# Performance work log

Hardware: AMD Instinct MI355X
Metric: run time of the kernel (lower is better)

## Reference

```python
import jax, jax.numpy as jnp
import numpy as np

B, S, F = 2, 2048, 2048
H, D = 16, 128  # F == H * D


def setup_inputs() -> dict:
    key = jax.random.key(0)
    k1, k2, k3 = jax.random.split(key, 3)
    x = jax.random.normal(k1, (B, S, F), dtype=jnp.float32)
    # causal attention mask, broadcast over batch and heads
    mask = jnp.tril(jnp.ones((S, S), dtype=bool))[None, None, :, :]
    init_std = 0.02
    c_attn_kernel = jax.random.normal(k2, (F, 3 * F), dtype=jnp.float32) * init_std
    c_attn_bias = jnp.zeros((3 * F,), dtype=jnp.float32)
    c_proj_kernel = jax.random.normal(k3, (F, F), dtype=jnp.float32) * init_std
    c_proj_bias = jnp.zeros((F,), dtype=jnp.float32)
    return {
        "x": x,
        "mask": mask,
        "c_attn_kernel": c_attn_kernel,
        "c_attn_bias": c_attn_bias,
        "c_proj_kernel": c_proj_kernel,
        "c_proj_bias": c_proj_bias,
    }


def reference(x, mask, c_attn_kernel, c_attn_bias, c_proj_kernel, c_proj_bias):
    dtype = x.dtype
    # fused QKV projection: [B,S,F] @ [F,3F] -> [B,S,3F]
    hidden = jnp.einsum('bsf,fe->bse', x, c_attn_kernel) + c_attn_bias
    q, k, v = jnp.split(hidden, 3, axis=-1)
    split = lambda t: t.reshape(t.shape[:-1] + (H, D))  # [B,S,H,D]
    q, k, v = split(q), split(k), split(v)
    q = q / jnp.sqrt(jnp.asarray(D, dtype))
    scores = jnp.einsum('bqhd,bkhd->bhqk', q, k)  # [B,H,S,S]
    big_neg = jnp.finfo(dtype).min
    scores = jnp.where(mask[..., :S, :S], scores, big_neg)
    weights = jax.nn.softmax(scores, axis=-1)
    z = jnp.einsum('bhqk,bkhd->bqhd', weights, v)  # [B,S,H,D]
    merged = z.reshape(z.shape[:-2] + (F,))  # [B,S,F]
    out = jnp.einsum('bsf,fe->bse', merged, c_proj_kernel) + c_proj_bias
    return out
```

## Files before the change

### kernel.cpp

```cpp
#include <hip/hip_runtime.h>
#include <hip/hip_bf16.h>
#include <stdint.h>

typedef __attribute__((ext_vector_type(8))) __bf16 bf16x8;
typedef __attribute__((ext_vector_type(4))) __bf16 bf16x4;
typedef __attribute__((ext_vector_type(4))) float f32x4;

#define DEV __device__ __forceinline__

static constexpr int S = 2048, F = 2048, H = 16, D = 128;
static constexpr int KDIM = F;
static constexpr float QSCALE = 0.08838834764831845f;

DEV void gll16(const void* g, void* l) {
  __builtin_amdgcn_global_load_lds(
      (const __attribute__((address_space(1))) void*)g,
      (__attribute__((address_space(3))) void*)l, 16, 0, 0);
}

DEV f32x4 mfma16(bf16x8 a, bf16x8 b, f32x4 c) {
  return __builtin_amdgcn_mfma_f32_16x16x32_bf16(a, b, c, 0, 0, 0);
}

extern __shared__ char smem[];

__global__ void k_cvt(const float* __restrict__ in, __bf16* __restrict__ out) {
  int i = blockIdx.x * 256 + threadIdx.x;
  float4 v = reinterpret_cast<const float4*>(in)[i];
  bf16x4 o = {(__bf16)v.x, (__bf16)v.y, (__bf16)v.z, (__bf16)v.w};
  reinterpret_cast<bf16x4*>(out)[i] = o;
}

__global__ void k_transpose(const float* __restrict__ in, __bf16* __restrict__ out,
                            int rows, int cols) {
  __shared__ float t[64][65];
  const int c0 = blockIdx.x * 64, r0 = blockIdx.y * 64;
  const int tx = threadIdx.x & 63, ty = threadIdx.x >> 6;
#pragma unroll
  for (int i = 0; i < 64; i += 4)
    t[ty + i][tx] = in[(size_t)(r0 + ty + i) * cols + c0 + tx];
  __syncthreads();
#pragma unroll
  for (int i = 0; i < 64; i += 4)
    out[(size_t)(c0 + ty + i) * rows + r0 + tx] = (__bf16)t[tx][ty + i];
}

template <int BM, int BN, int NBXL, int EPI>
__global__ __launch_bounds__(512, 1) void k_gp(
    const __bf16* __restrict__ A, const __bf16* __restrict__ Bt,
    const float* __restrict__ bias,
    __bf16* __restrict__ qo, __bf16* __restrict__ ko, __bf16* __restrict__ vo,
    float* __restrict__ fo) {
  constexpr int MF = BM / 32;
  constexpr int NF = BN / 64;
  constexpr int NH = NF / 2;
  constexpr int NLA = BM / 64;
  constexpr int NLB = BN / 64;
  constexpr int NL = NLA + NLB;
  constexpr int AOFF = BM * 128;
  constexpr int BUFSZ = (BM + BN) * 128;
  constexpr int NT = KDIM / 64;

  const int tid = threadIdx.x;
  const int lane = tid & 63, wid = tid >> 6;
  const int wm = wid >> 2, wn = wid & 3;
  const int ln = lane & 15, lm = lane >> 4;

  const int q8 = gridDim.x >> 3;
  const int lin = (blockIdx.x & 7) * q8 + (blockIdx.x >> 3);
  const int by = lin >> NBXL, bx = lin & ((1 << NBXL) - 1);
  const int mBase = by * BM, nBase = bx * BN;

  const int r0 = tid >> 3, cc = tid & 7;
  const int src0 = r0 * KDIM + ((cc ^ (r0 & 7)) << 3);
  const __bf16* Ab = A + (size_t)mBase * KDIM + src0;
  const __bf16* Bb = Bt + (size_t)nBase * KDIM + src0;
  const int dstBase = wid * 1024;

  auto stage = [&](char* buf, int t) {
    const __bf16* As = Ab + t * 64;
    const __bf16* Bs = Bb + t * 64;
#pragma unroll
    for (int j = 0; j < NLA; ++j)
      gll16(As + (size_t)j * 64 * KDIM, buf + j * 8192 + dstBase);
#pragma unroll
    for (int j = 0; j < NLB; ++j)
      gll16(Bs + (size_t)j * 64 * KDIM, buf + AOFF + j * 8192 + dstBase);
  };
  auto wait_nl = [&]() {
    if constexpr (NL == 4)       asm volatile("s_waitcnt vmcnt(4)" ::: "memory");
    else if constexpr (NL == 6)  asm volatile("s_waitcnt vmcnt(6)" ::: "memory");
    else if constexpr (NL == 8)  asm volatile("s_waitcnt vmcnt(8)" ::: "memory");
    else                         asm volatile("s_waitcnt vmcnt(10)" ::: "memory");
  };

  int rA[2], rB[2];
#pragma unroll
  for (int ks = 0; ks < 2; ++ks) {
    const int slot = (ks * 4 + lm) ^ (ln & 7);
    rA[ks] = (wm * (BM / 2) + ln) * 128 + slot * 16;
    rB[ks] = AOFF + (wn * (BN / 4) + ln) * 128 + slot * 16;
  }

  f32x4 acc[MF][NF] = {};

  stage(smem, 0);
  stage(smem + BUFSZ, 1);
  wait_nl();
  __builtin_amdgcn_s_barrier();
  __builtin_amdgcn_sched_barrier(0);

  for (int t = 0; t < NT; ++t) {
    char* cb = smem + (t & 1) * BUFSZ;
    bf16x8 a0[MF], a1[MF], b0[NF], b1[NF];

#pragma unroll
    for (int mi = 0; mi < MF; ++mi)
      a0[mi] = *reinterpret_cast<const bf16x8*>(cb + rA[0] + mi * 2048);
#pragma unroll
    for (int ni = 0; ni < NH; ++ni)
      b0[ni] = *reinterpret_cast<const bf16x8*>(cb + rB[0] + ni * 2048);
#pragma unroll
    for (int ni = NH; ni < NF; ++ni)
      b0[ni] = *reinterpret_cast<const bf16x8*>(cb + rB[0] + ni * 2048);

    __builtin_amdgcn_s_setprio(1);
#pragma unroll
    for (int ni = 0; ni < NH; ++ni)
#pragma unroll
      for (int mi = 0; mi < MF; ++mi)
        acc[mi][ni] = mfma16(a0[mi], b0[ni], acc[mi][ni]);
    __builtin_amdgcn_s_setprio(0);

#pragma unroll
    for (int mi = 0; mi < MF; ++mi)
      a1[mi] = *reinterpret_cast<const bf16x8*>(cb + rA[1] + mi * 2048);
#pragma unroll
    for (int ni = NH; ni < NF; ++ni)
      b1[ni] = *reinterpret_cast<const bf16x8*>(cb + rB[1] + ni * 2048);

    __builtin_amdgcn_s_setprio(1);
#pragma unroll
    for (int ni = NH; ni < NF; ++ni)
#pragma unroll
      for (int mi = 0; mi < MF; ++mi)
        acc[mi][ni] = mfma16(a0[mi], b0[ni], acc[mi][ni]);
    __builtin_amdgcn_s_setprio(0);

#pragma unroll
    for (int ni = 0; ni < NH; ++ni)
      b1[ni] = *reinterpret_cast<const bf16x8*>(cb + rB[1] + ni * 2048);

    __builtin_amdgcn_s_setprio(1);
#pragma unroll
    for (int ni = NH; ni < NF; ++ni)
#pragma unroll
      for (int mi = 0; mi < MF; ++mi)
        acc[mi][ni] = mfma16(a1[mi], b1[ni], acc[mi][ni]);
    __builtin_amdgcn_s_setprio(0);

    asm volatile("s_waitcnt lgkmcnt(0)" ::: "memory");
    __builtin_amdgcn_s_barrier();
    __builtin_amdgcn_sched_barrier(0);
    if (t + 2 < NT) stage(cb, t + 2);

    __builtin_amdgcn_s_setprio(1);
#pragma unroll
    for (int ni = 0; ni < NH; ++ni)
#pragma unroll
      for (int mi = 0; mi < MF; ++mi)
        acc[mi][ni] = mfma16(a1[mi], b1[ni], acc[mi][ni]);
    __builtin_amdgcn_s_setprio(0);

    if (t + 2 < NT) {
      wait_nl();
    } else if (t + 1 < NT) {
      asm volatile("s_waitcnt vmcnt(0)" ::: "memory");
    }
    if (t + 1 < NT) {
      __builtin_amdgcn_s_barrier();
      __builtin_amdgcn_sched_barrier(0);
    }
  }

  if (EPI == 0) {
#pragma unroll
    for (int mi = 0; mi < MF; ++mi) {
      const int grow = mBase + wm * (BM / 2) + mi * 16 + lm * 4;
      const int b = grow >> 11, s0 = grow & 2047;
#pragma unroll
      for (int ni = 0; ni < NF; ++ni) {
        const int gcol = nBase + wn * (BN / 4) + ni * 16 + ln;
        const float bv = bias[gcol];
        const int sec = gcol >> 11;
        const int h = (gcol >> 7) & 15, d = gcol & 127;
        const int bh = b * H + h;
        if (sec == 0) {
#pragma unroll
          for (int r = 0; r < 4; ++r)
            qo[((size_t)bh * S + s0 + r) * D + d] = (__bf16)((acc[mi][ni][r] + bv) * QSCALE);
        } else if (sec == 1) {
#pragma unroll
          for (int r = 0; r < 4; ++r)
            ko[((size_t)bh * S + s0 + r) * D + d] = (__bf16)(acc[mi][ni][r] + bv);
        } else {
          bf16x4 pv = {(__bf16)(acc[mi][ni][0] + bv), (__bf16)(acc[mi][ni][1] + bv),
                       (__bf16)(acc[mi][ni][2] + bv), (__bf16)(acc[mi][ni][3] + bv)};
          *reinterpret_cast<bf16x4*>(vo + ((size_t)bh * D + d) * S + s0) = pv;
        }
      }
    }
  } else {
#pragma unroll
    for (int mi = 0; mi < MF; ++mi) {
      const int grow = mBase + wm * (BM / 2) + mi * 16 + lm * 4;
#pragma unroll
      for (int ni = 0; ni < NF; ++ni) {
        const int gcol = nBase + wn * (BN / 4) + ni * 16 + ln;
        const float bv = bias[gcol];
#pragma unroll
        for (int r = 0; r < 4; ++r)
          fo[(size_t)(grow + r) * F + gcol] = acc[mi][ni][r] + bv;
      }
    }
  }
}

__global__ __launch_bounds__(256, 2) void k_attn(
    const __bf16* __restrict__ qb, const __bf16* __restrict__ kb,
    const __bf16* __restrict__ vtb, __bf16* __restrict__ zb) {
  const int lane = threadIdx.x & 63, w = threadIdx.x >> 6;
  const int lm = lane >> 4, ln = lane & 15;
  const int blk = blockIdx.x;
  const int u = blk & 255, v = blk >> 8;
  const int qt = v ? (u >> 4) : 15 - (u >> 4);
  const int bh = ((u & 15) << 1) | v;
  const int qw = qt * 128 + w * 32;

  const __bf16* qp = qb + (size_t)bh * S * D;
  const __bf16* kp = kb + (size_t)bh * S * D;
  const __bf16* vp = vtb + (size_t)bh * D * S;
  char* pw = smem + 65536 + w * 4096;

  int ksrc[4], kdst[4], vsrc[4], vdst[4];
#pragma unroll
  for (int j = 0; j < 4; ++j) {
    int c = (w * 4 + j) * 64 + lane;
    int kr = c >> 4, kps = (c & 15) ^ (kr & 7);
    ksrc[j] = kr * D + kps * 8;
    kdst[j] = (w * 4 + j) * 1024;
    int vr = c >> 3, vps = (c & 7) ^ (vr & 7);
    vsrc[j] = vr * S + vps * 8;
    vdst[j] = 16384 + (w * 4 + j) * 1024;
  }

  bf16x8 qf[2][4];
#pragma unroll
  for (int mi = 0; mi < 2; ++mi)
#pragma unroll
    for (int kf = 0; kf < 4; ++kf)
      qf[mi][kf] = *reinterpret_cast<const bf16x8*>(qp + (qw + mi * 16 + ln) * D + kf * 32 + lm * 8);

  f32x4 Oa[2][8] = {};
  float mrow[2][4], lrow[2][4];
#pragma unroll
  for (int mi = 0; mi < 2; ++mi)
#pragma unroll
    for (int r = 0; r < 4; ++r) { mrow[mi][r] = -3.0e38f; lrow[mi][r] = 0.0f; }

  const int ktEnd = 2 * qt + 1;

#pragma unroll
  for (int j = 0; j < 4; ++j) gll16(kp + ksrc[j], smem + kdst[j]);
#pragma unroll
  for (int j = 0; j < 4; ++j) gll16(vp + vsrc[j], smem + vdst[j]);
  asm volatile("s_waitcnt vmcnt(0)" ::: "memory");
  __builtin_amdgcn_s_barrier();
  __builtin_amdgcn_sched_barrier(0);

  for (int kt = 0; kt <= ktEnd; ++kt) {
    const int kv0 = kt * 64;
    const int cur = kt & 1;

    if (kt < ktEnd) {
      const int nk = (kt + 1) * 64;
      char* nbuf = smem + (cur ^ 1) * 32768;
#pragma unroll
      for (int j = 0; j < 4; ++j) gll16(kp + (size_t)nk * D + ksrc[j], nbuf + kdst[j]);
#pragma unroll
      for (int j = 0; j < 4; ++j) gll16(vp + nk + vsrc[j], nbuf + vdst[j]);
    }

    if (kv0 <= qw + 31) {
      const char* Kb = smem + cur * 32768;
      const char* Vb = Kb + 16384;
      const bool diag = (kv0 + 63 > qw);

      f32x4 sacc[2][4] = {};
#pragma unroll
      for (int kf = 0; kf < 4; ++kf) {
        bf16x8 kfr[4];
#pragma unroll
        for (int ni = 0; ni < 4; ++ni) {
          int row = ni * 16 + ln;
          int ch = (kf * 4 + lm) ^ (row & 7);
          kfr[ni] = *reinterpret_cast<const bf16x8*>(Kb + row * 256 + ch * 16);
        }
        __builtin_amdgcn_s_setprio(1);
#pragma unroll
        for (int mi = 0; mi < 2; ++mi)
#pragma unroll
          for (int ni = 0; ni < 4; ++ni)
            sacc[mi][ni] = mfma16(qf[mi][kf], kfr[ni], sacc[mi][ni]);
        __builtin_amdgcn_s_setprio(0);
      }

      if (diag) {
#pragma unroll
        for (int ni = 0; ni < 4; ++ni) {
          int c = kv0 + ni * 16 + ln;
#pragma unroll
          for (int mi = 0; mi < 2; ++mi) {
            int q0r = qw + mi * 16 + lm * 4;
#pragma unroll
            for (int r = 0; r < 4; ++r)
              if (c > q0r + r) sacc[mi][ni][r] = -1e30f;
          }
        }
      }

#pragma unroll
      for (int mi = 0; mi < 2; ++mi)
#pragma unroll
        for (int r = 0; r < 4; ++r) {
          float mx = fmaxf(fmaxf(sacc[mi][0][r], sacc[mi][1][r]),
                           fmaxf(sacc[mi][2][r], sacc[mi][3][r]));
          mx = fmaxf(mx, __shfl_xor(mx, 1, 64));
          mx = fmaxf(mx, __shfl_xor(mx, 2, 64));
          mx = fmaxf(mx, __shfl_xor(mx, 4, 64));
          mx = fmaxf(mx, __shfl_xor(mx, 8, 64));
          float mnew = fmaxf(mrow[mi][r], mx);
          float corr = __expf(mrow[mi][r] - mnew);
          mrow[mi][r] = mnew;
          float rs = 0.0f;
#pragma unroll
          for (int ni = 0; ni < 4; ++ni) {
            float p = __expf(sacc[mi][ni][r] - mnew);
            sacc[mi][ni][r] = p;
            rs += p;
          }
          lrow[mi][r] = lrow[mi][r] * corr + rs;
#pragma unroll
          for (int ni = 0; ni < 8; ++ni) Oa[mi][ni][r] *= corr;
        }

#pragma unroll
      for (int mi = 0; mi < 2; ++mi)
#pragma unroll
        for (int ni = 0; ni < 4; ++ni)
#pragma unroll
          for (int r = 0; r < 4; ++r) {
            int row = mi * 16 + lm * 4 + r;
            int bo = (row * 128 + (ni * 16 + ln) * 2) ^ ((row & 7) << 4);
            *reinterpret_cast<__bf16*>(pw + bo) = (__bf16)sacc[mi][ni][r];
          }

      asm volatile("s_waitcnt lgkmcnt(0)" ::: "memory");
      __builtin_amdgcn_sched_barrier(0);

#pragma unroll
      for (int kf = 0; kf < 2; ++kf) {
        bf16x8 pfr[2], vfr[8];
#pragma unroll
        for (int mi = 0; mi < 2; ++mi) {
          int row = mi * 16 + ln;
          int ch = (kf * 4 + lm) ^ (row & 7);
          pfr[mi] = *reinterpret_cast<const bf16x8*>(pw + row * 128 + ch * 16);
        }
#pragma unroll
        for (int ni = 0; ni < 8; ++ni) {
          int row = ni * 16 + ln;
          int ch = (kf * 4 + lm) ^ (row & 7);
          vfr[ni] = *reinterpret_cast<const bf16x8*>(Vb + row * 128 + ch * 16);
        }
        __builtin_amdgcn_s_setprio(1);
#pragma unroll
        for (int mi = 0; mi < 2; ++mi)
#pragma unroll
          for (int ni = 0; ni < 8; ++ni)
            Oa[mi][ni] = mfma16(pfr[mi], vfr[ni], Oa[mi][ni]);
        __builtin_amdgcn_s_setprio(0);
      }
    }

    asm volatile("s_waitcnt vmcnt(0) lgkmcnt(0)" ::: "memory");
    __builtin_amdgcn_s_barrier();
    __builtin_amdgcn_sched_barrier(0);
  }

#pragma unroll
  for (int mi = 0; mi < 2; ++mi)
#pragma unroll
    for (int r = 0; r < 4; ++r) {
      float ls = lrow[mi][r];
      ls += __shfl_xor(ls, 1, 64);
      ls += __shfl_xor(ls, 2, 64);
      ls += __shfl_xor(ls, 4, 64);
      ls += __shfl_xor(ls, 8, 64);
      lrow[mi][r] = 1.0f / ls;
    }
  const int b = bh >> 4, h = bh & 15;
#pragma unroll
  for (int mi = 0; mi < 2; ++mi)
#pragma unroll
    for (int ni = 0; ni < 8; ++ni) {
      int d = ni * 16 + ln;
#pragma unroll
      for (int r = 0; r < 4; ++r) {
        int qrow = qw + mi * 16 + lm * 4 + r;
        zb[(size_t)(b * S + qrow) * F + h * D + d] = (__bf16)(Oa[mi][ni][r] * lrow[mi][r]);
      }
    }
}

extern "C" void kernel_launch(void* const* d_in, const int* in_sizes, int n_in,
                              void* d_out, int out_size, void* d_ws, size_t ws_size,
                              hipStream_t stream) {
  const float* x = (const float*)d_in[0];
  const float* w_attn = (const float*)d_in[2];
  const float* b_attn = (const float*)d_in[3];
  const float* w_proj = (const float*)d_in[4];
  const float* b_proj = (const float*)d_in[5];
  float* out = (float*)d_out;

  char* ws = (char*)d_ws;
  __bf16* xb    = (__bf16*)(ws + 0);
  __bf16* wqkv  = (__bf16*)(ws + 16777216);
  __bf16* wpro  = (__bf16*)(ws + 41943040);
  __bf16* qb    = (__bf16*)(ws + 50331648);
  __bf16* kb    = (__bf16*)(ws + 67108864);
  __bf16* vtb   = (__bf16*)(ws + 83886080);
  __bf16* zb    = xb;

  (void)hipFuncSetAttribute((const void*)k_gp<128, 384, 4, 0>,
                            hipFuncAttributeMaxDynamicSharedMemorySize, 131072);
  (void)hipFuncSetAttribute((const void*)k_gp<128, 256, 3, 1>,
                            hipFuncAttributeMaxDynamicSharedMemorySize, 98304);
  (void)hipFuncSetAttribute((const void*)k_attn,
                            hipFuncAttributeMaxDynamicSharedMemorySize, 81920);

  k_cvt<<<8192, 256, 0, stream>>>(x, xb);
  k_transpose<<<dim3(96, 32), 256, 0, stream>>>(w_attn, wqkv, 2048, 6144);
  k_transpose<<<dim3(32, 32), 256, 0, stream>>>(w_proj, wpro, 2048, 2048);
  k_gp<128, 384, 4, 0><<<512, 512, 131072, stream>>>(xb, wqkv, b_attn, qb, kb, vtb, nullptr);
  k_attn<<<512, 256, 81920, stream>>>(qb, kb, vtb, zb);
  k_gp<128, 256, 3, 1><<<256, 512, 98304, stream>>>(zb, wpro, b_proj, nullptr, nullptr, nullptr, out);
}
```

Measured before the change: 258.9 us.

## Add 256x256-tile QKV GEMM with 8-phase interleaved load/MFMA schedule

Replaces the QKV projection GEMM (previously 128x384 tiles, 512 blocks) with a dedicated kernel using 256x256 tiles over 384 blocks. Global-to-LDS loads are split into half-tile pieces, and each piece is issued between MFMA phases with fine-grained barriers and vmcnt waits, so loads overlap compute across a double buffer. The larger tile raises operand reuse per LDS read, and 384 blocks avoids a partial second wave. The cost is more barriers per K step and a hand-tuned wait-count schedule that is fragile. The rest of the changes are macro refactors and removal of the now-unused epilogue template parameter.

```diff
diff --git a/kernel.cpp b/kernel.cpp
--- a/kernel.cpp
+++ b/kernel.cpp
@@ -45,12 +45,172 @@
     out[(size_t)(c0 + ty + i) * rows + r0 + tx] = (__bf16)t[tx][ty + i];
 }
 
-template <int BM, int BN, int NBXL, int EPI>
+template <int MH>
+DEV void mmq(f32x4 (&acc)[8][4], const bf16x8 (&a)[4], const bf16x8 (&b)[4]) {
+#pragma unroll
+  for (int ni = 0; ni < 4; ++ni)
+#pragma unroll
+    for (int mi = 0; mi < 4; ++mi)
+      acc[MH * 4 + mi][ni] = mfma16(a[mi], b[ni], acc[MH * 4 + mi][ni]);
+}
+
+#define QBAR()  __builtin_amdgcn_s_barrier()
+#define QLGKM() asm volatile("s_waitcnt lgkmcnt(0)" ::: "memory")
+#define QSCB()  __builtin_amdgcn_sched_barrier(0)
+
+__global__ __launch_bounds__(512, 1) void k_qkv8(
+    const __bf16* __restrict__ A, const __bf16* __restrict__ Bt,
+    const float* __restrict__ bias,
+    __bf16* __restrict__ qo, __bf16* __restrict__ ko, __bf16* __restrict__ vo) {
+  constexpr int NT = 32;
+
+  const int tid = threadIdx.x;
+  const int lane = tid & 63, wid = tid >> 6;
+  const int wm = wid >> 2, wn = wid & 3;
+  const int ln = lane & 15, lm = lane >> 4;
+
+  const int lin = (blockIdx.x & 7) * 48 + (blockIdx.x >> 3);
+  const int by = lin / 24, bx = lin % 24;
+  const int mBase = by * 256, nBase = bx * 256;
+
+  const int r0 = tid >> 3, cc = tid & 7;
+  const int src0 = r0 * KDIM + ((cc ^ (r0 & 7)) << 3);
+  const __bf16* Ab = A + (size_t)mBase * KDIM + src0;
+  const __bf16* Bb = Bt + (size_t)nBase * KDIM + src0;
+  const int sDst = wid * 1024;
+
+  auto stA = [&](int t, int h) {
+    char* d = smem + (t & 1) * 65536 + h * 16384 + sDst;
+    const __bf16* s = Ab + (size_t)(h * 128) * KDIM + t * 64;
+    gll16(s, d);
+    gll16(s + (size_t)64 * KDIM, d + 8192);
+  };
+  auto stB = [&](int t, int h) {
+    char* d = smem + (t & 1) * 65536 + 32768 + h * 16384 + sDst;
+    const __bf16* s = Bb + (size_t)(h * 128) * KDIM + t * 64;
+    gll16(s, d);
+    gll16(s + (size_t)64 * KDIM, d + 8192);
+  };
+
+  int aOff[2], bOff[2];
+#pragma unroll
+  for (int ks = 0; ks < 2; ++ks) {
+    const int slot = (ks * 4 + lm) ^ (ln & 7);
+    aOff[ks] = (wm * 128 + ln) * 128 + slot * 16;
+    bOff[ks] = 32768 + (wn * 64 + ln) * 128 + slot * 16;
+  }
+  auto rdA = [&](bf16x8 (&a)[4], const char* rb, int mh, int ks) {
+#pragma unroll
+    for (int mi = 0; mi < 4; ++mi)
+      a[mi] = *reinterpret_cast<const bf16x8*>(rb + aOff[ks] + (mh * 4 + mi) * 2048);
+  };
+  auto rdB = [&](bf16x8 (&b)[4], const char* rb, int ks) {
+#pragma unroll
+    for (int ni = 0; ni < 4; ++ni)
+      b[ni] = *reinterpret_cast<const bf16x8*>(rb + bOff[ks] + ni * 2048);
+  };
+
+  f32x4 acc[8][4] = {};
+
+  stA(0, 0); stA(0, 1); stB(0, 0); stB(0, 1); stB(1, 0);
+  asm volatile("s_waitcnt vmcnt(2)" ::: "memory");
+  QBAR(); QSCB();
+
+  for (int i = 0; i < 16; ++i) {
+    const char* L = smem;
+    const char* R = smem + 65536;
+    const int t1 = 2 * i + 1, t2 = 2 * i + 2, t3 = 2 * i + 3;
+    const bool last = (i == 15);
+    bf16x8 a[4], b0[4], b1[4];
+
+    rdA(a, L, 0, 0); rdB(b0, L, 0);
+    stA(t1, 0);
+    QBAR(); QLGKM(); QSCB();
+    __builtin_amdgcn_s_setprio(1); mmq<0>(acc, a, b0); __builtin_amdgcn_s_setprio(0);
+    QBAR(); QSCB();
+
+    rdA(a, L, 1, 0);
+    stA(t1, 1);
+    QBAR(); QLGKM(); QSCB();
+    __builtin_amdgcn_s_setprio(1); mmq<1>(acc, a, b0); __builtin_amdgcn_s_setprio(0);
+    asm volatile("s_waitcnt vmcnt(6)" ::: "memory");
+    QBAR(); QSCB();
+
+    rdA(a, L, 0, 1); rdB(b1, L, 1);
+    stB(t1, 1);
+    QBAR(); QLGKM(); QSCB();
+    __builtin_amdgcn_s_setprio(1); mmq<0>(acc, a, b1); __builtin_amdgcn_s_setprio(0);
+    QBAR(); QSCB();
+
+    rdA(a, L, 1, 1);
+    if (t2 < NT) stB(t2, 0);
+    QBAR(); QLGKM(); QSCB();
+    __builtin_amdgcn_s_setprio(1); mmq<1>(acc, a, b1); __builtin_amdgcn_s_setprio(0);
+    if (last) asm volatile("s_waitcnt vmcnt(0)" ::: "memory");
+    else      asm volatile("s_waitcnt vmcnt(4)" ::: "memory");
+    QBAR(); QSCB();
+
+    rdA(a, R, 0, 0); rdB(b0, R, 0);
+    if (t2 < NT) stA(t2, 0);
+    QBAR(); QLGKM(); QSCB();
+    __builtin_amdgcn_s_setprio(1); mmq<0>(acc, a, b0); __builtin_amdgcn_s_setprio(0);
+    QBAR(); QSCB();
+
+    rdA(a, R, 1, 0);
+    if (t2 < NT) stA(t2, 1);
+    QBAR(); QLGKM(); QSCB();
+    __builtin_amdgcn_s_setprio(1); mmq<1>(acc, a, b0); __builtin_amdgcn_s_setprio(0);
+    asm volatile("s_waitcnt vmcnt(6)" ::: "memory");
+    QBAR(); QSCB();
+
+    rdA(a, R, 0, 1); rdB(b1, R, 1);
+    if (t2 < NT) stB(t2, 1);
+    QBAR(); QLGKM(); QSCB();
+    __builtin_amdgcn_s_setprio(1); mmq<0>(acc, a, b1); __builtin_amdgcn_s_setprio(0);
+    QBAR(); QSCB();
+
+    rdA(a, R, 1, 1);
+    if (t3 < NT) stB(t3, 0);
+    QBAR(); QLGKM(); QSCB();
+    __builtin_amdgcn_s_setprio(1); mmq<1>(acc, a, b1); __builtin_amdgcn_s_setprio(0);
+    if (!last) {
+      asm volatile("s_waitcnt vmcnt(4)" ::: "memory");
+      QBAR(); QSCB();
+    }
+  }
+
+  const int sec = nBase >> 11;
+#pragma unroll
+  for (int mi = 0; mi < 8; ++mi) {
+    const int grow = mBase + wm * 128 + mi * 16 + lm * 4;
+    const int b = grow >> 11, s0 = grow & 2047;
+#pragma unroll
+    for (int ni = 0; ni < 4; ++ni) {
+      const int gcol = nBase + wn * 64 + ni * 16 + ln;
+      const float bv = bias[gcol];
+      const int h = (gcol >> 7) & 15, d = gcol & 127;
+      const int bh = b * H + h;
+      if (sec == 0) {
+#pragma unroll
+        for (int r = 0; r < 4; ++r)
+          qo[((size_t)bh * S + s0 + r) * D + d] = (__bf16)((acc[mi][ni][r] + bv) * QSCALE);
+      } else if (sec == 1) {
+#pragma unroll
+        for (int r = 0; r < 4; ++r)
+          ko[((size_t)bh * S + s0 + r) * D + d] = (__bf16)(acc[mi][ni][r] + bv);
+      } else {
+        bf16x4 pv = {(__bf16)(acc[mi][ni][0] + bv), (__bf16)(acc[mi][ni][1] + bv),
+                     (__bf16)(acc[mi][ni][2] + bv), (__bf16)(acc[mi][ni][3] + bv)};
+        *reinterpret_cast<bf16x4*>(vo + ((size_t)bh * D + d) * S + s0) = pv;
+      }
+    }
+  }
+}
+
+template <int BM, int BN, int NBXL>
 __global__ __launch_bounds__(512, 1) void k_gp(
     const __bf16* __restrict__ A, const __bf16* __restrict__ Bt,
-    const float* __restrict__ bias,
-    __bf16* __restrict__ qo, __bf16* __restrict__ ko, __bf16* __restrict__ vo,
-    float* __restrict__ fo) {
+    const float* __restrict__ bias, float* __restrict__ fo) {
   constexpr int MF = BM / 32;
   constexpr int NF = BN / 64;
   constexpr int NH = NF / 2;
@@ -90,8 +250,7 @@
   auto wait_nl = [&]() {
     if constexpr (NL == 4)       asm volatile("s_waitcnt vmcnt(4)" ::: "memory");
     else if constexpr (NL == 6)  asm volatile("s_waitcnt vmcnt(6)" ::: "memory");
-    else if constexpr (NL == 8)  asm volatile("s_waitcnt vmcnt(8)" ::: "memory");
-    else                         asm volatile("s_waitcnt vmcnt(10)" ::: "memory");
+    else                         asm volatile("s_waitcnt vmcnt(8)" ::: "memory");
   };
 
   int rA[2], rB[2];
@@ -107,8 +266,7 @@
   stage(smem, 0);
   stage(smem + BUFSZ, 1);
   wait_nl();
-  __builtin_amdgcn_s_barrier();
-  __builtin_amdgcn_sched_barrier(0);
+  QBAR(); QSCB();
 
   for (int t = 0; t < NT; ++t) {
     char* cb = smem + (t & 1) * BUFSZ;
@@ -118,10 +276,7 @@
     for (int mi = 0; mi < MF; ++mi)
       a0[mi] = *reinterpret_cast<const bf16x8*>(cb + rA[0] + mi * 2048);
 #pragma unroll
-    for (int ni = 0; ni < NH; ++ni)
-      b0[ni] = *reinterpret_cast<const bf16x8*>(cb + rB[0] + ni * 2048);
-#pragma unroll
-    for (int ni = NH; ni < NF; ++ni)
+    for (int ni = 0; ni < NF; ++ni)
       b0[ni] = *reinterpret_cast<const bf16x8*>(cb + rB[0] + ni * 2048);
 
     __builtin_amdgcn_s_setprio(1);
@@ -159,9 +314,8 @@
         acc[mi][ni] = mfma16(a1[mi], b1[ni], acc[mi][ni]);
     __builtin_amdgcn_s_setprio(0);
 
-    asm volatile("s_waitcnt lgkmcnt(0)" ::: "memory");
-    __builtin_amdgcn_s_barrier();
-    __builtin_amdgcn_sched_barrier(0);
+    QLGKM();
+    QBAR(); QSCB();
     if (t + 2 < NT) stage(cb, t + 2);
 
     __builtin_amdgcn_s_setprio(1);
@@ -178,50 +332,20 @@
       asm volatile("s_waitcnt vmcnt(0)" ::: "memory");
     }
     if (t + 1 < NT) {
-      __builtin_amdgcn_s_barrier();
-      __builtin_amdgcn_sched_barrier(0);
-    }
-  }
-
-  if (EPI == 0) {
-#pragma unroll
-    for (int mi = 0; mi < MF; ++mi) {
-      const int grow = mBase + wm * (BM / 2) + mi * 16 + lm * 4;
-      const int b = grow >> 11, s0 = grow & 2047;
-#pragma unroll
-      for (int ni = 0; ni < NF; ++ni) {
-        const int gcol = nBase + wn * (BN / 4) + ni * 16 + ln;
-        const float bv = bias[gcol];
-        const int sec = gcol >> 11;
-        const int h = (gcol >> 7) & 15, d = gcol & 127;
-        const int bh = b * H + h;
-        if (sec == 0) {
-#pragma unroll
-          for (int r = 0; r < 4; ++r)
-            qo[((size_t)bh * S + s0 + r) * D + d] = (__bf16)((acc[mi][ni][r] + bv) * QSCALE);
-        } else if (sec == 1) {
-#pragma unroll
-          for (int r = 0; r < 4; ++r)
-            ko[((size_t)bh * S + s0 + r) * D + d] = (__bf16)(acc[mi][ni][r] + bv);
-        } else {
-          bf16x4 pv = {(__bf16)(acc[mi][ni][0] + bv), (__bf16)(acc[mi][ni][1] + bv),
-                       (__bf16)(acc[mi][ni][2] + bv), (__bf16)(acc[mi][ni][3] + bv)};
-          *reinterpret_cast<bf16x4*>(vo + ((size_t)bh * D + d) * S + s0) = pv;
-        }
-      }
-    }
-  } else {
-#pragma unroll
-    for (int mi = 0; mi < MF; ++mi) {
-      const int grow = mBase + wm * (BM / 2) + mi * 16 + lm * 4;
-#pragma unroll
-      for (int ni = 0; ni < NF; ++ni) {
-        const int gcol = nBase + wn * (BN / 4) + ni * 16 + ln;
-        const float bv = bias[gcol];
-#pragma unroll
-        for (int r = 0; r < 4; ++r)
-          fo[(size_t)(grow + r) * F + gcol] = acc[mi][ni][r] + bv;
-      }
+      QBAR(); QSCB();
+    }
+  }
+
+#pragma unroll
+  for (int mi = 0; mi < MF; ++mi) {
+    const int grow = mBase + wm * (BM / 2) + mi * 16 + lm * 4;
+#pragma unroll
+    for (int ni = 0; ni < NF; ++ni) {
+      const int gcol = nBase + wn * (BN / 4) + ni * 16 + ln;
+      const float bv = bias[gcol];
+#pragma unroll
+      for (int r = 0; r < 4; ++r)
+        fo[(size_t)(grow + r) * F + gcol] = acc[mi][ni][r] + bv;
     }
   }
 }
@@ -275,8 +399,7 @@
 #pragma unroll
   for (int j = 0; j < 4; ++j) gll16(vp + vsrc[j], smem + vdst[j]);
   asm volatile("s_waitcnt vmcnt(0)" ::: "memory");
-  __builtin_amdgcn_s_barrier();
-  __builtin_amdgcn_sched_barrier(0);
+  QBAR(); QSCB();
 
   for (int kt = 0; kt <= ktEnd; ++kt) {
     const int kv0 = kt * 64;
@@ -365,8 +488,7 @@
             *reinterpret_cast<__bf16*>(pw + bo) = (__bf16)sacc[mi][ni][r];
           }
 
-      asm volatile("s_waitcnt lgkmcnt(0)" ::: "memory");
-      __builtin_amdgcn_sched_barrier(0);
+      QLGKM(); QSCB();
 
 #pragma unroll
       for (int kf = 0; kf < 2; ++kf) {
@@ -394,8 +516,7 @@
     }
 
     asm volatile("s_waitcnt vmcnt(0) lgkmcnt(0)" ::: "memory");
-    __builtin_amdgcn_s_barrier();
-    __builtin_amdgcn_sched_barrier(0);
+    QBAR(); QSCB();
   }
 
 #pragma unroll
@@ -442,9 +563,9 @@
   __bf16* vtb   = (__bf16*)(ws + 83886080);
   __bf16* zb    = xb;
 
-  (void)hipFuncSetAttribute((const void*)k_gp<128, 384, 4, 0>,
+  (void)hipFuncSetAttribute((const void*)k_qkv8,
                             hipFuncAttributeMaxDynamicSharedMemorySize, 131072);
-  (void)hipFuncSetAttribute((const void*)k_gp<128, 256, 3, 1>,
+  (void)hipFuncSetAttribute((const void*)k_gp<128, 256, 3>,
                             hipFuncAttributeMaxDynamicSharedMemorySize, 98304);
   (void)hipFuncSetAttribute((const void*)k_attn,
                             hipFuncAttributeMaxDynamicSharedMemorySize, 81920);
@@ -452,7 +573,7 @@
   k_cvt<<<8192, 256, 0, stream>>>(x, xb);
   k_transpose<<<dim3(96, 32), 256, 0, stream>>>(w_attn, wqkv, 2048, 6144);
   k_transpose<<<dim3(32, 32), 256, 0, stream>>>(w_proj, wpro, 2048, 2048);
-  k_gp<128, 384, 4, 0><<<512, 512, 131072, stream>>>(xb, wqkv, b_attn, qb, kb, vtb, nullptr);
+  k_qkv8<<<384, 512, 131072, stream>>>(xb, wqkv, b_attn, qb, kb, vtb);
   k_attn<<<512, 256, 81920, stream>>>(qb, kb, vtb, zb);
-  k_gp<128, 256, 3, 1><<<256, 512, 98304, stream>>>(zb, wpro, b_proj, nullptr, nullptr, nullptr, out);
-}
+  k_gp<128, 256, 3><<<256, 512, 98304, stream>>>(zb, wpro, b_proj, out);
+}
```

Measured after the change: 270.9 us. 4.6% more time.

## Prefetch K/V two tiles ahead and skip softmax rescale unless max grows

Applied to the files above, without the earlier changes.

Restructures the attention inner loop so K/V tiles are issued two iterations ahead, using partial vmcnt waits so a full tile of loads overlaps compute instead of one. It also applies lazy online-softmax rescaling: the running max and the output/denominator correction are only updated when some row's new max exceeds the old by more than 8, which saves exp and multiply work on most tiles. The price is an extra barrier per iteration. The unrescaled exponentials can reach about e^8, which bf16 P and fp32 accumulators tolerate.

```diff
diff --git a/kernel.cpp b/kernel.cpp
--- a/kernel.cpp
+++ b/kernel.cpp
@@ -253,6 +253,14 @@
     vsrc[j] = vr * S + vps * 8;
     vdst[j] = 16384 + (w * 4 + j) * 1024;
   }
+  auto stage = [&](int kt) {
+    char* buf = smem + (kt & 1) * 32768;
+    const int kv = kt * 64;
+#pragma unroll
+    for (int j = 0; j < 4; ++j) gll16(kp + (size_t)kv * D + ksrc[j], buf + kdst[j]);
+#pragma unroll
+    for (int j = 0; j < 4; ++j) gll16(vp + kv + vsrc[j], buf + vdst[j]);
+  };
 
   bf16x8 qf[2][4];
 #pragma unroll
@@ -270,30 +278,19 @@
 
   const int ktEnd = 2 * qt + 1;
 
-#pragma unroll
-  for (int j = 0; j < 4; ++j) gll16(kp + ksrc[j], smem + kdst[j]);
-#pragma unroll
-  for (int j = 0; j < 4; ++j) gll16(vp + vsrc[j], smem + vdst[j]);
-  asm volatile("s_waitcnt vmcnt(0)" ::: "memory");
+  stage(0);
+  stage(1);
+  asm volatile("s_waitcnt vmcnt(8)" ::: "memory");
   __builtin_amdgcn_s_barrier();
   __builtin_amdgcn_sched_barrier(0);
 
   for (int kt = 0; kt <= ktEnd; ++kt) {
     const int kv0 = kt * 64;
     const int cur = kt & 1;
-
-    if (kt < ktEnd) {
-      const int nk = (kt + 1) * 64;
-      char* nbuf = smem + (cur ^ 1) * 32768;
-#pragma unroll
-      for (int j = 0; j < 4; ++j) gll16(kp + (size_t)nk * D + ksrc[j], nbuf + kdst[j]);
-#pragma unroll
-      for (int j = 0; j < 4; ++j) gll16(vp + nk + vsrc[j], nbuf + vdst[j]);
-    }
+    const char* Kb = smem + cur * 32768;
+    const char* Vb = Kb + 16384;
 
     if (kv0 <= qw + 31) {
-      const char* Kb = smem + cur * 32768;
-      const char* Vb = Kb + 16384;
       const bool diag = (kv0 + 63 > qw);
 
       f32x4 sacc[2][4] = {};
@@ -329,6 +326,8 @@
         }
       }
 
+      float mx_[2][4];
+      bool big = false;
 #pragma unroll
       for (int mi = 0; mi < 2; ++mi)
 #pragma unroll
@@ -339,19 +338,34 @@
           mx = fmaxf(mx, __shfl_xor(mx, 2, 64));
           mx = fmaxf(mx, __shfl_xor(mx, 4, 64));
           mx = fmaxf(mx, __shfl_xor(mx, 8, 64));
-          float mnew = fmaxf(mrow[mi][r], mx);
-          float corr = __expf(mrow[mi][r] - mnew);
-          mrow[mi][r] = mnew;
+          mx_[mi][r] = mx;
+          big = big || (mx > mrow[mi][r] + 8.0f);
+        }
+      if (__any((int)big)) {
+#pragma unroll
+        for (int mi = 0; mi < 2; ++mi)
+#pragma unroll
+          for (int r = 0; r < 4; ++r) {
+            float mnew = fmaxf(mrow[mi][r], mx_[mi][r]);
+            float corr = __expf(mrow[mi][r] - mnew);
+            mrow[mi][r] = mnew;
+            lrow[mi][r] *= corr;
+#pragma unroll
+            for (int ni = 0; ni < 8; ++ni) Oa[mi][ni][r] *= corr;
+          }
+      }
+#pragma unroll
+      for (int mi = 0; mi < 2; ++mi)
+#pragma unroll
+        for (int r = 0; r < 4; ++r) {
           float rs = 0.0f;
 #pragma unroll
           for (int ni = 0; ni < 4; ++ni) {
-            float p = __expf(sacc[mi][ni][r] - mnew);
+            float p = __expf(sacc[mi][ni][r] - mrow[mi][r]);
             sacc[mi][ni][r] = p;
             rs += p;
           }
-          lrow[mi][r] = lrow[mi][r] * corr + rs;
-#pragma unroll
-          for (int ni = 0; ni < 8; ++ni) Oa[mi][ni][r] *= corr;
+          lrow[mi][r] += rs;
         }
 
 #pragma unroll
@@ -393,9 +407,18 @@
       }
     }
 
-    asm volatile("s_waitcnt vmcnt(0) lgkmcnt(0)" ::: "memory");
+    asm volatile("s_waitcnt lgkmcnt(0)" ::: "memory");
     __builtin_amdgcn_s_barrier();
     __builtin_amdgcn_sched_barrier(0);
+    if (kt + 2 <= ktEnd) stage(kt + 2);
+    if (kt + 1 <= ktEnd) {
+      if (kt + 2 <= ktEnd)
+        asm volatile("s_waitcnt vmcnt(8)" ::: "memory");
+      else
+        asm volatile("s_waitcnt vmcnt(0)" ::: "memory");
+      __builtin_amdgcn_s_barrier();
+      __builtin_amdgcn_sched_barrier(0);
+    }
   }
 
 #pragma unroll
```

Measured after the change: 262.9 us. No clear change (+1.5%).
